# Performance work log

Hardware: AMD Instinct MI355X
Metric: run time of the kernel (lower is better)

The kernel has to match this reference:

```python
import jax, jax.numpy as jnp
import numpy as np

N, E, D, H = 50000, 800000, 128, 128


def _uniform_param(key, shape, fan_in):
    bound = 1.0 / np.sqrt(fan_in)
    return jax.random.uniform(key, shape, jnp.float32, -bound, bound)


def setup_inputs() -> dict:
    key = jax.random.key(0)
    ks = jax.random.split(key, 12)
    x = jax.random.normal(ks[0], (N, D), jnp.float32)
    xedge = jax.random.randint(ks[1], (2, E), 0, N, jnp.int64)
    y = jax.random.randint(ks[2], (N,), 0, 2, jnp.int32).astype(bool)
    return {
        "x": x,
        "xedge": xedge,
        "y": y,
        "pretrain": 0,
        # SAGEConv layer 1 (in=D, out=H): lin_l (with bias) applied to mean aggr, lin_r (no bias) to self
        "W1l": _uniform_param(ks[3], (D, H), D),
        "b1l": _uniform_param(ks[4], (H,), D),
        "W1r": _uniform_param(ks[5], (D, H), D),
        # SAGEConv layer 2 (in=H, out=H)
        "W2l": _uniform_param(ks[6], (H, H), H),
        "b2l": _uniform_param(ks[7], (H,), H),
        "W2r": _uniform_param(ks[8], (H, H), H),
        # Decoder weight [H, H]
        "Wdec": _uniform_param(ks[9], (H, H), H),
    }


def sage_conv(h, src, dst, Wl, bl, Wr, num_nodes):
    # gather neighbor features along edges, mean-aggregate by destination
    msgs = h[src]                                            # [E, d]
    agg = jax.ops.segment_sum(msgs, dst, num_segments=num_nodes)
    cnt = jax.ops.segment_sum(jnp.ones((src.shape[0],), h.dtype), dst,
                              num_segments=num_nodes)
    mean = agg / jnp.maximum(cnt, 1.0)[:, None]              # [N, d]
    return mean @ Wl + bl + h @ Wr                           # [N, out]


def reference(x, xedge, y, pretrain, W1l, b1l, W1r, W2l, b2l, W2r, Wdec):
    src, dst = xedge[0], xedge[1]
    n = x.shape[0]
    # Encoder: SAGE = conv1 -> relu -> (dropout: eval identity) -> conv2
    h = jax.nn.relu(sage_conv(x, src, dst, W1l, b1l, W1r, n))
    emb = sage_conv(h, src, dst, W2l, b2l, W2r, n)           # [N, H]
    # Decoder
    dx = emb @ Wdec                                          # [N, H]
    # BCEWithLogits: pos nodes target 1, neg nodes target 0, mean within each group
    ym = y.astype(dx.dtype)                                  # [N]
    n_pos = jnp.sum(ym)
    n_neg = n - n_pos
    hdim = dx.shape[1]
    sp_pos = jax.nn.softplus(-dx)   # bce(logit, 1)
    sp_neg = jax.nn.softplus(dx)    # bce(logit, 0)
    l2 = jnp.sum(sp_pos * ym[:, None]) / (jnp.maximum(n_pos, 1.0) * hdim)
    l1 = jnp.sum(sp_neg * (1.0 - ym)[:, None]) / (jnp.maximum(n_neg, 1.0) * hdim)
    return (l1 + l2, emb)
```

## Files before the change

kernel.cpp:

```cpp
#include <hip/hip_runtime.h>
#include <hip/hip_bf16.h>

#define NDIM 128
#define MROWS 32
#define BTHREADS 512
#define SCAN_CHUNK 1024

typedef __attribute__((ext_vector_type(8))) short short8;
typedef __attribute__((ext_vector_type(4))) float f32x4;

__device__ __forceinline__ float bf2f(__hip_bfloat16 v) { return __bfloat162float(v); }

__device__ __forceinline__ float ldf(const void* p, long i, int f32) {
    return f32 ? ((const float*)p)[i] : bf2f(((const __hip_bfloat16*)p)[i]);
}
__device__ __forceinline__ void stf(void* p, long i, int f32, float v) {
    if (f32) ((float*)p)[i] = v;
    else     ((__hip_bfloat16*)p)[i] = __float2bfloat16(v);
}
__device__ __forceinline__ short f2bf(float v) {
    __hip_bfloat16 h = __float2bfloat16(v);
    short s;
    __builtin_memcpy(&s, &h, 2);
    return s;
}
__device__ __forceinline__ float bflo(unsigned u) { u <<= 16; float f; __builtin_memcpy(&f, &u, 4); return f; }
__device__ __forceinline__ float bfhi(unsigned u) { u &= 0xffff0000u; float f; __builtin_memcpy(&f, &u, 4); return f; }
__device__ __forceinline__ unsigned packbf(float a, float b) {
    unsigned la = (unsigned short)f2bf(a);
    unsigned hb = (unsigned short)f2bf(b);
    return (hb << 16) | la;
}
__device__ __forceinline__ int aswz(int m, int k) {
    return m * NDIM + ((((k >> 3) ^ (m & 7)) << 3) | (k & 7));
}
__device__ __forceinline__ int wswz(int m, int p) {
    return m * 64 + ((((p >> 2) ^ (m & 7)) << 2) | (p & 3));
}

#define GLOAD(dst, sa, voff)                                              \
    asm volatile("global_load_dword %0, %1, %2"                           \
                 : "=v"(dst) : "v"(voff), "s"(sa) : "memory")


__global__ void prep_kernel(const void* __restrict__ x,
                            const void* __restrict__ W1l, const void* __restrict__ b1l,
                            const void* __restrict__ W1r, const void* __restrict__ W2l,
                            const void* __restrict__ b2l, const void* __restrict__ W2r,
                            const void* __restrict__ Wd,
                            short* __restrict__ T1l, short* __restrict__ T1r,
                            short* __restrict__ T2l, short* __restrict__ T2r,
                            short* __restrict__ Td, float* __restrict__ b1c,
                            float* __restrict__ b2c, unsigned* __restrict__ xb,
                            const int* __restrict__ xedge, int E,
                            int* __restrict__ cnt, int N,
                            int* __restrict__ flags) {
    __shared__ int s_se, s_sc;
    const int t = threadIdx.x;
    if (t == 0) { s_se = 1; s_sc = 0; }
    __syncthreads();
    {
        for (int i = t; i < 512; i += 256)
            if (xedge[2 * i + 1] != 0) s_se = 0;
        const unsigned short* xh = (const unsigned short*)x;
        int c = 0;
        for (int i = t; i < 1024; i += 256) {
            int ex = (xh[2 * i] >> 7) & 0xFF;
            if (ex >= 100 && ex <= 150) c++;
        }
        atomicAdd(&s_sc, c);
    }
    __syncthreads();
    const int e64 = s_se;
    const int wf = (s_sc < 900) ? 1 : 0;
    if (blockIdx.x == 0 && t == 0) {
        flags[0] = e64;
        flags[2] = wf;
    }
    const long idx = (long)blockIdx.x * 256 + t;
    if (idx < E) {
        int d = e64 ? xedge[2 * (E + idx)] : xedge[E + idx];
        atomicAdd(&cnt[d], 1);
    }
    if (idx < NDIM * NDIM) {
        int k = (int)(idx >> 7), n = (int)(idx & 127);
        int o = n * NDIM + k;
        T1l[o] = f2bf(ldf(W1l, idx, wf));
        T1r[o] = f2bf(ldf(W1r, idx, wf));
        T2l[o] = f2bf(ldf(W2l, idx, wf));
        T2r[o] = f2bf(ldf(W2r, idx, wf));
        Td [o] = f2bf(ldf(Wd , idx, wf));
        if (idx < NDIM) { b1c[idx] = ldf(b1l, idx, wf); b2c[idx] = ldf(b2l, idx, wf); }
    }
    if (wf) {
        const long np = (long)N * 64;
        const long stride = (long)gridDim.x * 256;
        for (long pidx = idx; pidx < np; pidx += stride) {
            float2 v = ((const float2*)x)[pidx];
            xb[pidx] = packbf(v.x, v.y);
        }
    }
}


__global__ void scan_partial(const int* __restrict__ cnt, int* __restrict__ bsum, int N,
                             const unsigned int* __restrict__ yw,
                             int* __restrict__ flags) {
    __shared__ int red[256];
    const int t = threadIdx.x;
    if (blockIdx.x == 0) {
        __shared__ int s_sy;
        if (t == 0) s_sy = 0;
        __syncthreads();
        for (int i = t; i < 1024; i += 256)
            if (yw[i] > 1u) s_sy = 1;
        __syncthreads();
        if (t == 0) flags[1] = s_sy;
    }
    const long base = (long)blockIdx.x * SCAN_CHUNK + (long)t * 4;
    int s = 0;
#pragma unroll
    for (int i = 0; i < 4; ++i) { long idx = base + i; if (idx < N) s += cnt[idx]; }
    red[t] = s;
    __syncthreads();
    for (int off = 128; off >= 1; off >>= 1) {
        if (t < off) red[t] += red[t + off];
        __syncthreads();
    }
    if (t == 0) bsum[blockIdx.x] = red[0];
}

__global__ void scan_scatter(int* __restrict__ cnt, const int* __restrict__ bsum,
                             int* __restrict__ rowptr, int N) {
    __shared__ int tsum[256];
    __shared__ int red[256];
    const int t = threadIdx.x;
    const long base = (long)blockIdx.x * SCAN_CHUNK + (long)t * 4;
    int loc[4];
    int s = 0;
#pragma unroll
    for (int i = 0; i < 4; ++i) {
        long idx = base + i;
        int c = (idx < N) ? cnt[idx] : 0;
        loc[i] = s;
        s += c;
    }
    tsum[t] = s;
    int sown = 0;
    for (int i = t; i < blockIdx.x; i += 256) sown += bsum[i];
    red[t] = sown;
    __syncthreads();
    for (int off = 1; off < 256; off <<= 1) {
        int u = (t >= off) ? tsum[t - off] : 0;
        __syncthreads();
        tsum[t] += u;
        __syncthreads();
    }
    for (int off = 128; off >= 1; off >>= 1) {
        if (t < off) red[t] += red[t + off];
        __syncthreads();
    }
    const int b0 = red[0];
    const int texcl = tsum[t] - s;
#pragma unroll
    for (int i = 0; i < 4; ++i) {
        long idx = base + i;
        if (idx < N) {
            int v = b0 + texcl + loc[i];
            rowptr[idx] = v;
            cnt[idx] = v;
        }
    }
    if (blockIdx.x == gridDim.x - 1 && t == 255) rowptr[N] = b0 + tsum[255];
}

__global__ void fill_kernel(const int* __restrict__ xedge, int E,
                            const int* __restrict__ flags,
                            int* __restrict__ cur, int* __restrict__ col) {
    int e = blockIdx.x * blockDim.x + threadIdx.x;
    if (e >= E) return;
    const int e64 = flags[0];
    int s = e64 ? xedge[2 * e] : xedge[e];
    int d = e64 ? xedge[2 * (E + e)] : xedge[E + e];
    int p = atomicAdd(&cur[d], 1);
    col[p] = s;
}


template <bool RELU, int OUTMODE>
__global__ __launch_bounds__(BTHREADS, 2)
void layer_mfma(const unsigned* __restrict__ Xb, const unsigned* __restrict__ Xraw,
                const int* __restrict__ rowptr,
                const int* __restrict__ col, const short* __restrict__ WlT,
                const float* __restrict__ biasc, const short* __restrict__ WrT,
                const short* __restrict__ WdT, const void* __restrict__ yv,
                const int* __restrict__ flags, void* __restrict__ outp,
                float* __restrict__ accum, int* __restrict__ npos, int N) {
    __shared__ short AS[2 * MROWS * NDIM];
    __shared__ int ylds[MROWS];
    __shared__ float redm[8][2];
    short* Ms = AS;
    short* Ss = AS + MROWS * NDIM;
    unsigned* Msw = (unsigned*)Ms;
    unsigned* Ssw = (unsigned*)Ss;
    const int t = threadIdx.x;
    const int n0 = blockIdx.x * MROWS;
    const int wf = flags[2];
    const unsigned* __restrict__ X = wf ? Xb : Xraw;

    if (OUTMODE == 1 && t < MROWS) {
        const int yb = flags[1];
        int n = n0 + t;
        int yn = -1;
        if (n < N)
            yn = yb ? (int)((const unsigned char*)yv)[n]
                    : (((const int*)yv)[n] != 0 ? 1 : 0);
        ylds[t] = yn;
    }

    {
        const int p = t & 63;
        const unsigned voff = (unsigned)(p * 4);
        const unsigned long long Xb64 = (unsigned long long)(uintptr_t)X;
        const int g = __builtin_amdgcn_readfirstlane(t >> 6);
        int r = g;
        int b = 0, e = 0;
        {
            int n = n0 + r;
            if (n < N) {
                b = __builtin_amdgcn_readfirstlane(rowptr[n]);
                e = __builtin_amdgcn_readfirstlane(rowptr[n + 1]);
            }
        }
        for (int it = 0; it < 4; ++it, r += 8) {
            const int n = n0 + r;
            const int deg = e - b;
            const int* colb = col + b;
            int cs[32];
            if (deg > 0) {
#pragma unroll
                for (int j = 0; j < 8; ++j) {
                    int c = __builtin_amdgcn_readfirstlane(colb[j]);
                    cs[j] = ((unsigned)c >= (unsigned)N) ? 0 : c;
                }
            }
            if (deg > 8) {
#pragma unroll
                for (int j = 8; j < 16; ++j) {
                    int c = __builtin_amdgcn_readfirstlane(colb[j]);
                    cs[j] = ((unsigned)c >= (unsigned)N) ? 0 : c;
                }
            }
            if (deg > 16) {
#pragma unroll
                for (int j = 16; j < 24; ++j) {
                    int c = __builtin_amdgcn_readfirstlane(colb[j]);
                    cs[j] = ((unsigned)c >= (unsigned)N) ? 0 : c;
                }
            }
            if (deg > 24) {
#pragma unroll
                for (int j = 24; j < 32; ++j) {
                    int c = __builtin_amdgcn_readfirstlane(colb[j]);
                    cs[j] = ((unsigned)c >= (unsigned)N) ? 0 : c;
                }
            }
            int bn = 0, en = 0;
            if (it < 3) {
                int nn = n0 + r + 8;
                if (nn < N) {
                    bn = __builtin_amdgcn_readfirstlane(rowptr[nn]);
                    en = __builtin_amdgcn_readfirstlane(rowptr[nn + 1]);
                }
            }
            unsigned u[32];
            unsigned su = 0;
            if (n < N) {
                unsigned long long sa = Xb64 + ((unsigned long long)(unsigned)n << 8);
                GLOAD(su, sa, voff);
            }
            if (deg > 0) {
#pragma unroll
                for (int j = 0; j < 8; ++j) {
                    unsigned long long sa = Xb64 + ((unsigned long long)(unsigned)cs[j] << 8);
                    GLOAD(u[j], sa, voff);
                }
            }
            if (deg > 8) {
#pragma unroll
                for (int j = 8; j < 16; ++j) {
                    unsigned long long sa = Xb64 + ((unsigned long long)(unsigned)cs[j] << 8);
                    GLOAD(u[j], sa, voff);
                }
            }
            if (deg > 16) {
#pragma unroll
                for (int j = 16; j < 24; ++j) {
                    unsigned long long sa = Xb64 + ((unsigned long long)(unsigned)cs[j] << 8);
                    GLOAD(u[j], sa, voff);
                }
            }
            if (deg > 24) {
#pragma unroll
                for (int j = 24; j < 32; ++j) {
                    unsigned long long sa = Xb64 + ((unsigned long long)(unsigned)cs[j] << 8);
                    GLOAD(u[j], sa, voff);
                }
            }
            asm volatile("s_waitcnt vmcnt(0)" ::: "memory");
            __builtin_amdgcn_sched_barrier(0);
            if (n < N) asm volatile("" : "+v"(su));
            if (deg > 0) {
#pragma unroll
                for (int j = 0; j < 8; ++j) asm volatile("" : "+v"(u[j]));
            }
            if (deg > 8) {
#pragma unroll
                for (int j = 8; j < 16; ++j) asm volatile("" : "+v"(u[j]));
            }
            if (deg > 16) {
#pragma unroll
                for (int j = 16; j < 24; ++j) asm volatile("" : "+v"(u[j]));
            }
            if (deg > 24) {
#pragma unroll
                for (int j = 24; j < 32; ++j) asm volatile("" : "+v"(u[j]));
            }
            float m0 = 0.f, m1 = 0.f;
            if (deg > 0) {
                float p0 = 0.f, p1 = 0.f, p2 = 0.f, p3 = 0.f;
                float q0 = 0.f, q1 = 0.f, q2 = 0.f, q3 = 0.f;
#pragma unroll
                for (int j = 0; j < 32; j += 4) {
                    if (j + 0 < deg) { p0 += bflo(u[j]);     q0 += bfhi(u[j]); }
                    if (j + 1 < deg) { p1 += bflo(u[j + 1]); q1 += bfhi(u[j + 1]); }
                    if (j + 2 < deg) { p2 += bflo(u[j + 2]); q2 += bfhi(u[j + 2]); }
                    if (j + 3 < deg) { p3 += bflo(u[j + 3]); q3 += bfhi(u[j + 3]); }
                }
                m0 = (p0 + p1) + (p2 + p3);
                m1 = (q0 + q1) + (q2 + q3);
                for (int i = b + 32; i < e; ++i) {
                    int c = __builtin_amdgcn_readfirstlane(col[i]);
                    unsigned uu = X[(long)c * 64 + p];
                    m0 += bflo(uu);
                    m1 += bfhi(uu);
                }
                float inv = 1.f / (float)deg;
                m0 *= inv; m1 *= inv;
            }
            int wi = wswz(r, p);
            Msw[wi] = packbf(m0, m1);
            Ssw[wi] = su;
            b = bn; e = en;
        }
    }
    __syncthreads();
    const int l = t & 63, w = t >> 6;
    const int quad = l >> 4, l15 = l & 15;
    const int wcol = w * 16;
    f32x4 acc[2] = {};
    for (int k0 = 0; k0 < NDIM; k0 += 32) {
        const int kc = k0 + quad * 8;
        short8 ams[2], ass[2], bl, br;
#pragma unroll
        for (int rt = 0; rt < 2; ++rt) {
            int m = rt * 16 + l15;
            ams[rt] = *(const short8*)&Ms[aswz(m, kc)];
            ass[rt] = *(const short8*)&Ss[aswz(m, kc)];
        }
        {
            int n = wcol + l15;
            bl = *(const short8*)&WlT[n * NDIM + kc];
            br = *(const short8*)&WrT[n * NDIM + kc];
        }
#pragma unroll
        for (int rt = 0; rt < 2; ++rt) {
            acc[rt] = __builtin_amdgcn_mfma_f32_16x16x32_bf16(
                ams[rt], bl, acc[rt], 0, 0, 0);
            acc[rt] = __builtin_amdgcn_mfma_f32_16x16x32_bf16(
                ass[rt], br, acc[rt], 0, 0, 0);
        }
    }
    __syncthreads();

    if (OUTMODE == 0) {
        {
            int cg = wcol + l15;
            float bv = biasc[cg];
#pragma unroll
            for (int rt = 0; rt < 2; ++rt)
#pragma unroll
                for (int reg = 0; reg < 4; ++reg) {
                    int row = rt * 16 + quad * 4 + reg;
                    float v = acc[rt][reg] + bv;
                    if (RELU) v = fmaxf(v, 0.f);
                    Ms[row * NDIM + cg] = f2bf(v);
                }
        }
        __syncthreads();
        unsigned* ob = (unsigned*)outp;
        for (int idx = t; idx < MROWS * 64; idx += BTHREADS) {
            int r = idx >> 6;
            if (n0 + r < N) ob[(long)n0 * 64 + idx] = Msw[idx];
        }
    } else {
        {
            int cg = wcol + l15;
            float bv = biasc[cg];
#pragma unroll
            for (int rt = 0; rt < 2; ++rt)
#pragma unroll
                for (int reg = 0; reg < 4; ++reg) {
                    int row = rt * 16 + quad * 4 + reg;
                    float v = acc[rt][reg] + bv;
                    Ms[aswz(row, cg)] = f2bf(v);
                    int n = n0 + row;
                    if (n < N) {
                        if (wf) ((float*)outp)[1 + (long)n * NDIM + cg] = v;
                        else ((__hip_bfloat16*)outp)[1 + (long)n * NDIM + cg] =
                                 __float2bfloat16(v);
                    }
                }
        }
        __syncthreads();
        f32x4 acc2[2] = {};
        for (int k0 = 0; k0 < NDIM; k0 += 32) {
            const int kc = k0 + quad * 8;
            short8 a[2], bwd;
#pragma unroll
            for (int rt = 0; rt < 2; ++rt)
                a[rt] = *(const short8*)&Ms[aswz(rt * 16 + l15, kc)];
            bwd = *(const short8*)&WdT[(wcol + l15) * NDIM + kc];
#pragma unroll
            for (int rt = 0; rt < 2; ++rt)
                acc2[rt] = __builtin_amdgcn_mfma_f32_16x16x32_bf16(
                    a[rt], bwd, acc2[rt], 0, 0, 0);
        }
        float lpos = 0.f, lneg = 0.f;
#pragma unroll
        for (int rt = 0; rt < 2; ++rt)
#pragma unroll
            for (int reg = 0; reg < 4; ++reg) {
                int row = rt * 16 + quad * 4 + reg;
                int yn = ylds[row];
                if (yn >= 0) {
                    float z = acc2[rt][reg];
                    float L = log1pf(expf(-fabsf(z)));
                    if (yn) lpos += fmaxf(-z, 0.f) + L;
                    else    lneg += fmaxf(z, 0.f) + L;
                }
            }
#pragma unroll
        for (int off = 32; off >= 1; off >>= 1) {
            lpos += __shfl_down(lpos, off, 64);
            lneg += __shfl_down(lneg, off, 64);
        }
        if (l == 0) { redm[w][0] = lpos; redm[w][1] = lneg; }
        __syncthreads();
        if (t == 0) {
            float sp = 0.f, sn = 0.f;
#pragma unroll
            for (int i = 0; i < 8; ++i) { sp += redm[i][0]; sn += redm[i][1]; }
            atomicAdd(&accum[0], sp);
            atomicAdd(&accum[1], sn);
            int c = 0;
            for (int i = 0; i < MROWS; ++i) if (ylds[i] > 0) c++;
            if (c) atomicAdd(npos, c);
        }
    }
}

__global__ void finalize_kernel(const float* __restrict__ accum, const int* __restrict__ npos,
                                const int* __restrict__ flags, void* __restrict__ out, int N) {
    float np_ = (float)(*npos);
    float nn_ = (float)N - np_;
    float l2 = accum[0] / (fmaxf(np_, 1.f) * 128.f);
    float l1 = accum[1] / (fmaxf(nn_, 1.f) * 128.f);
    stf(out, 0, flags[2], l1 + l2);
}


extern "C" void kernel_launch(void* const* d_in, const int* in_sizes, int n_in,
                              void* d_out, int out_size, void* d_ws, size_t ws_size,
                              hipStream_t stream) {
    const void* x    = d_in[0];
    const int* xedge = (const int*)d_in[1];
    const void* y    = d_in[2];
    const void* W1l  = d_in[4];
    const void* b1l  = d_in[5];
    const void* W1r  = d_in[6];
    const void* W2l  = d_in[7];
    const void* b2l  = d_in[8];
    const void* W2r  = d_in[9];
    const void* Wdec = d_in[10];

    const int N = in_sizes[0] / NDIM;
    const int E = in_sizes[1] / 2;

    char* ws = (char*)d_ws;
    size_t off = 0;
    auto alloc = [&](size_t bytes) -> void* {
        void* p = ws + off;
        off = (off + bytes + 255) & ~(size_t)255;
        return p;
    };
    int*   flags  = (int*)alloc(64);
    int*   cnt    = (int*)alloc((size_t)N * 4);
    float* accum  = (float*)alloc(64);
    int*   npos   = (int*)alloc(64);
    int*   bsum   = (int*)alloc(1024 * 4);
    int*   rowptr = (int*)alloc((size_t)(N + 1) * 4);
    int*   col    = (int*)alloc((size_t)E * 4);
    unsigned* xb  = (unsigned*)alloc((size_t)N * 64 * 4);
    unsigned* hbuf = (unsigned*)alloc((size_t)N * 64 * 4);
    short* T1l = (short*)alloc(NDIM * NDIM * 2);
    short* T1r = (short*)alloc(NDIM * NDIM * 2);
    short* T2l = (short*)alloc(NDIM * NDIM * 2);
    short* T2r = (short*)alloc(NDIM * NDIM * 2);
    short* Td  = (short*)alloc(NDIM * NDIM * 2);
    float* b1c = (float*)alloc(NDIM * 4);
    float* b2c = (float*)alloc(NDIM * 4);

    const size_t zlen = (((size_t)N * 4 + 255) & ~(size_t)255) + 512;
    hipMemsetAsync(cnt, 0, zlen, stream);

    const long prep_items = (E > NDIM * NDIM) ? E : NDIM * NDIM;
    prep_kernel<<<(int)((prep_items + 255) / 256), 256, 0, stream>>>(
        x, W1l, b1l, W1r, W2l, b2l, W2r, Wdec,
        T1l, T1r, T2l, T2r, Td, b1c, b2c, xb, xedge, E, cnt, N, flags);

    const int sb = (N + SCAN_CHUNK - 1) / SCAN_CHUNK;
    scan_partial<<<sb, 256, 0, stream>>>(cnt, bsum, N, (const unsigned int*)y, flags);
    scan_scatter<<<sb, 256, 0, stream>>>(cnt, bsum, rowptr, N);

    const int eb = (E + 255) / 256;
    fill_kernel<<<eb, 256, 0, stream>>>(xedge, E, flags, cnt, col);

    const int nbM = (N + MROWS - 1) / MROWS;
    layer_mfma<true, 0><<<nbM, BTHREADS, 0, stream>>>(
        xb, (const unsigned*)x, rowptr, col, T1l, b1c, T1r, nullptr, nullptr,
        flags, hbuf, nullptr, nullptr, N);
    layer_mfma<false, 1><<<nbM, BTHREADS, 0, stream>>>(
        hbuf, hbuf, rowptr, col, T2l, b2c, T2r, Td, y, flags,
        d_out, accum, npos, N);
    finalize_kernel<<<1, 1, 0, stream>>>(accum, npos, flags, d_out, N);
}
```

Baseline: 308.0 us.

## Fuse graph preprocessing into one cooperative kernel and fold finalize into last block

Replaces the memset, prep, two scan kernels and fill kernel with a single cooperative kernel of 1024 blocks. It uses grid-wide syncs between the degree-count, prefix-sum and CSR-fill phases. The separate finalize kernel is removed: the last block to finish the second layer, found through an atomic done counter, computes the loss. This cuts launch count and inter-kernel gaps, at the cost of grid.sync overhead, a serial per-block prefix loop, and relying on the cooperative launch succeeding (there is a fallback path).

```diff
diff --git a/kernel.cpp b/kernel.cpp
--- a/kernel.cpp
+++ b/kernel.cpp
@@ -1,10 +1,14 @@
 #include <hip/hip_runtime.h>
 #include <hip/hip_bf16.h>
+#include <hip/hip_cooperative_groups.h>
+
+namespace cg = cooperative_groups;
 
 #define NDIM 128
 #define MROWS 32
 #define BTHREADS 512
 #define SCAN_CHUNK 1024
+#define COOP_G 1024
 
 typedef __attribute__((ext_vector_type(8))) short short8;
 typedef __attribute__((ext_vector_type(4))) float f32x4;
@@ -41,6 +45,149 @@
 #define GLOAD(dst, sa, voff)                                              \
     asm volatile("global_load_dword %0, %1, %2"                           \
                  : "=v"(dst) : "v"(voff), "s"(sa) : "memory")
+
+__device__ __forceinline__ void detect_flags(const int* xedge, const void* x,
+                                             int* s_se, int* s_sc,
+                                             int* e64_out, int* wf_out) {
+    const int t = threadIdx.x;
+    if (t == 0) { *s_se = 1; *s_sc = 0; }
+    __syncthreads();
+    for (int i = t; i < 512; i += 256)
+        if (xedge[2 * i + 1] != 0) *s_se = 0;
+    {
+        const unsigned short* xh = (const unsigned short*)x;
+        int c = 0;
+        for (int i = t; i < 1024; i += 256) {
+            int ex = (xh[2 * i] >> 7) & 0xFF;
+            if (ex >= 100 && ex <= 150) c++;
+        }
+        atomicAdd(s_sc, c);
+    }
+    __syncthreads();
+    *e64_out = *s_se;
+    *wf_out = (*s_sc < 900) ? 1 : 0;
+}
+
+
+__global__ __launch_bounds__(256, 4)
+void coop_build(const void* __restrict__ x,
+                const void* __restrict__ W1l, const void* __restrict__ b1l,
+                const void* __restrict__ W1r, const void* __restrict__ W2l,
+                const void* __restrict__ b2l, const void* __restrict__ W2r,
+                const void* __restrict__ Wd,
+                short* __restrict__ T1l, short* __restrict__ T1r,
+                short* __restrict__ T2l, short* __restrict__ T2r,
+                short* __restrict__ Td, float* __restrict__ b1c,
+                float* __restrict__ b2c, unsigned* __restrict__ xb,
+                const int* __restrict__ xedge, int E,
+                int* __restrict__ cnt, int N,
+                int* __restrict__ flags, float* __restrict__ accum,
+                int* __restrict__ npos, int* __restrict__ donecnt,
+                int* __restrict__ gpart, int* __restrict__ rowptr,
+                int* __restrict__ col, const unsigned int* __restrict__ yw) {
+    cg::grid_group grid = cg::this_grid();
+    const int t = threadIdx.x;
+    const int b = blockIdx.x;
+    const long gid = (long)b * 256 + t;
+    const long gstride = (long)gridDim.x * 256;
+
+    __shared__ int s_se, s_sc;
+    int e64, wf;
+    detect_flags(xedge, x, &s_se, &s_sc, &e64, &wf);
+    if (b == 0) {
+        if (t == 0) {
+            flags[0] = e64; flags[2] = wf;
+            atomicExch((int*)&accum[0], 0);
+            atomicExch((int*)&accum[1], 0);
+            atomicExch(npos, 0);
+            atomicExch(donecnt, 0);
+        }
+        __shared__ int s_sy;
+        if (t == 0) s_sy = 0;
+        __syncthreads();
+        for (int i = t; i < 1024; i += 256)
+            if (yw[i] > 1u) s_sy = 1;
+        __syncthreads();
+        if (t == 0) flags[1] = s_sy;
+    }
+    for (long i = gid; i < N; i += gstride) atomicExch(&cnt[i], 0);
+    for (long i = gid; i < NDIM * NDIM; i += gstride) {
+        int k = (int)(i >> 7), n = (int)(i & 127);
+        int o = n * NDIM + k;
+        T1l[o] = f2bf(ldf(W1l, i, wf));
+        T1r[o] = f2bf(ldf(W1r, i, wf));
+        T2l[o] = f2bf(ldf(W2l, i, wf));
+        T2r[o] = f2bf(ldf(W2r, i, wf));
+        Td [o] = f2bf(ldf(Wd , i, wf));
+        if (i < NDIM) { b1c[i] = ldf(b1l, i, wf); b2c[i] = ldf(b2l, i, wf); }
+    }
+    if (wf) {
+        const long np = (long)N * 64;
+        for (long p = gid; p < np; p += gstride) {
+            float2 v = ((const float2*)x)[p];
+            xb[p] = packbf(v.x, v.y);
+        }
+    }
+    grid.sync();
+    for (long e = gid; e < E; e += gstride) {
+        int d = e64 ? xedge[2 * (E + e)] : xedge[E + e];
+        atomicAdd(&cnt[d], 1);
+    }
+    grid.sync();
+    const int C = (N + gridDim.x - 1) / gridDim.x;
+    __shared__ int red[256];
+    __shared__ int sc_[1024];
+    {
+        int s = 0;
+        for (int i = t; i < C; i += 256) {
+            long idx = (long)b * C + i;
+            if (idx < N) s += atomicAdd(&cnt[idx], 0);
+        }
+        red[t] = s;
+        __syncthreads();
+        for (int off = 128; off >= 1; off >>= 1) {
+            if (t < off) red[t] += red[t + off];
+            __syncthreads();
+        }
+        if (t == 0) atomicExch(&gpart[b], red[0]);
+    }
+    grid.sync();
+    {
+        int sown = 0;
+        for (int i = t; i < b; i += 256) sown += atomicAdd(&gpart[i], 0);
+        red[t] = sown;
+        __syncthreads();
+        for (int off = 128; off >= 1; off >>= 1) {
+            if (t < off) red[t] += red[t + off];
+            __syncthreads();
+        }
+        const int base = red[0];
+        for (int i = t; i < C; i += 256) {
+            long idx = (long)b * C + i;
+            sc_[i] = (idx < N) ? atomicAdd(&cnt[idx], 0) : 0;
+        }
+        __syncthreads();
+        if (t == 0) {
+            int run = base;
+            for (int i = 0; i < C; ++i) {
+                long idx = (long)b * C + i;
+                if (idx < N) {
+                    rowptr[idx] = run;
+                    atomicExch(&cnt[idx], run);
+                    run += sc_[i];
+                }
+            }
+        }
+        if (b == 0 && t == 0) rowptr[N] = E;
+    }
+    grid.sync();
+    for (long e = gid; e < E; e += gstride) {
+        int s_ = e64 ? xedge[2 * e] : xedge[e];
+        int d  = e64 ? xedge[2 * (E + e)] : xedge[E + e];
+        int p = atomicAdd(&cnt[d], 1);
+        col[p] = s_;
+    }
+}
 
 
 __global__ void prep_kernel(const void* __restrict__ x,
@@ -57,26 +204,9 @@
                             int* __restrict__ flags) {
     __shared__ int s_se, s_sc;
     const int t = threadIdx.x;
-    if (t == 0) { s_se = 1; s_sc = 0; }
-    __syncthreads();
-    {
-        for (int i = t; i < 512; i += 256)
-            if (xedge[2 * i + 1] != 0) s_se = 0;
-        const unsigned short* xh = (const unsigned short*)x;
-        int c = 0;
-        for (int i = t; i < 1024; i += 256) {
-            int ex = (xh[2 * i] >> 7) & 0xFF;
-            if (ex >= 100 && ex <= 150) c++;
-        }
-        atomicAdd(&s_sc, c);
-    }
-    __syncthreads();
-    const int e64 = s_se;
-    const int wf = (s_sc < 900) ? 1 : 0;
-    if (blockIdx.x == 0 && t == 0) {
-        flags[0] = e64;
-        flags[2] = wf;
-    }
+    int e64, wf;
+    detect_flags(xedge, x, &s_se, &s_sc, &e64, &wf);
+    if (blockIdx.x == 0 && t == 0) { flags[0] = e64; flags[2] = wf; }
     const long idx = (long)blockIdx.x * 256 + t;
     if (idx < E) {
         int d = e64 ? xedge[2 * (E + idx)] : xedge[E + idx];
@@ -101,7 +231,6 @@
         }
     }
 }
-
 
 __global__ void scan_partial(const int* __restrict__ cnt, int* __restrict__ bsum, int N,
                              const unsigned int* __restrict__ yw,
@@ -195,7 +324,8 @@
                 const float* __restrict__ biasc, const short* __restrict__ WrT,
                 const short* __restrict__ WdT, const void* __restrict__ yv,
                 const int* __restrict__ flags, void* __restrict__ outp,
-                float* __restrict__ accum, int* __restrict__ npos, int N) {
+                float* __restrict__ accum, int* __restrict__ npos,
+                int* __restrict__ donecnt, int N) {
     __shared__ short AS[2 * MROWS * NDIM];
     __shared__ int ylds[MROWS];
     __shared__ float redm[8][2];
@@ -466,17 +596,20 @@
             int c = 0;
             for (int i = 0; i < MROWS; ++i) if (ylds[i] > 0) c++;
             if (c) atomicAdd(npos, c);
-        }
-    }
-}
-
-__global__ void finalize_kernel(const float* __restrict__ accum, const int* __restrict__ npos,
-                                const int* __restrict__ flags, void* __restrict__ out, int N) {
-    float np_ = (float)(*npos);
-    float nn_ = (float)N - np_;
-    float l2 = accum[0] / (fmaxf(np_, 1.f) * 128.f);
-    float l1 = accum[1] / (fmaxf(nn_, 1.f) * 128.f);
-    stf(out, 0, flags[2], l1 + l2);
+            __threadfence();
+            unsigned d = (unsigned)atomicAdd(donecnt, 1);
+            if (d == (unsigned)(gridDim.x - 1)) {
+                float spT = atomicAdd(&accum[0], 0.f);
+                float snT = atomicAdd(&accum[1], 0.f);
+                int npv = atomicAdd(npos, 0);
+                float np_ = (float)npv;
+                float nn_ = (float)N - np_;
+                float l2v = spT / (fmaxf(np_, 1.f) * 128.f);
+                float l1v = snT / (fmaxf(nn_, 1.f) * 128.f);
+                stf(outp, 0, wf, l1v + l2v);
+            }
+        }
+    }
 }
 
 
@@ -508,7 +641,8 @@
     int*   cnt    = (int*)alloc((size_t)N * 4);
     float* accum  = (float*)alloc(64);
     int*   npos   = (int*)alloc(64);
-    int*   bsum   = (int*)alloc(1024 * 4);
+    int*   donecnt= (int*)alloc(64);
+    int*   gpart  = (int*)alloc((size_t)COOP_G * 4);
     int*   rowptr = (int*)alloc((size_t)(N + 1) * 4);
     int*   col    = (int*)alloc((size_t)E * 4);
     unsigned* xb  = (unsigned*)alloc((size_t)N * 64 * 4);
@@ -521,27 +655,42 @@
     float* b1c = (float*)alloc(NDIM * 4);
     float* b2c = (float*)alloc(NDIM * 4);
 
-    const size_t zlen = (((size_t)N * 4 + 255) & ~(size_t)255) + 512;
-    hipMemsetAsync(cnt, 0, zlen, stream);
-
-    const long prep_items = (E > NDIM * NDIM) ? E : NDIM * NDIM;
-    prep_kernel<<<(int)((prep_items + 255) / 256), 256, 0, stream>>>(
-        x, W1l, b1l, W1r, W2l, b2l, W2r, Wdec,
-        T1l, T1r, T2l, T2r, Td, b1c, b2c, xb, xedge, E, cnt, N, flags);
-
-    const int sb = (N + SCAN_CHUNK - 1) / SCAN_CHUNK;
-    scan_partial<<<sb, 256, 0, stream>>>(cnt, bsum, N, (const unsigned int*)y, flags);
-    scan_scatter<<<sb, 256, 0, stream>>>(cnt, bsum, rowptr, N);
-
-    const int eb = (E + 255) / 256;
-    fill_kernel<<<eb, 256, 0, stream>>>(xedge, E, flags, cnt, col);
+    bool coop_ok = (N <= COOP_G * 1024);
+    if (coop_ok) {
+        const void* xv = x;
+        int Ev = E, Nv = N;
+        void* args[] = {
+            (void*)&xv, (void*)&W1l, (void*)&b1l, (void*)&W1r, (void*)&W2l,
+            (void*)&b2l, (void*)&W2r, (void*)&Wdec,
+            (void*)&T1l, (void*)&T1r, (void*)&T2l, (void*)&T2r, (void*)&Td,
+            (void*)&b1c, (void*)&b2c, (void*)&xb, (void*)&xedge, (void*)&Ev,
+            (void*)&cnt, (void*)&Nv, (void*)&flags, (void*)&accum,
+            (void*)&npos, (void*)&donecnt, (void*)&gpart, (void*)&rowptr,
+            (void*)&col, (void*)&y };
+        hipError_t err = hipLaunchCooperativeKernel(
+            (const void*)coop_build, dim3(COOP_G), dim3(256), args, 0, stream);
+        if (err != hipSuccess) coop_ok = false;
+    }
+    if (!coop_ok) {
+        const size_t zlen = (((size_t)N * 4 + 255) & ~(size_t)255) + 3 * 256;
+        hipMemsetAsync(cnt, 0, zlen, stream);
+        const long prep_items = (E > NDIM * NDIM) ? E : NDIM * NDIM;
+        prep_kernel<<<(int)((prep_items + 255) / 256), 256, 0, stream>>>(
+            x, W1l, b1l, W1r, W2l, b2l, W2r, Wdec,
+            T1l, T1r, T2l, T2r, Td, b1c, b2c, xb, xedge, E, cnt, N, flags);
+        const int sb = (N + SCAN_CHUNK - 1) / SCAN_CHUNK;
+        scan_partial<<<sb, 256, 0, stream>>>(cnt, gpart, N,
+                                             (const unsigned int*)y, flags);
+        scan_scatter<<<sb, 256, 0, stream>>>(cnt, gpart, rowptr, N);
+        const int eb = (E + 255) / 256;
+        fill_kernel<<<eb, 256, 0, stream>>>(xedge, E, flags, cnt, col);
+    }
 
     const int nbM = (N + MROWS - 1) / MROWS;
     layer_mfma<true, 0><<<nbM, BTHREADS, 0, stream>>>(
         xb, (const unsigned*)x, rowptr, col, T1l, b1c, T1r, nullptr, nullptr,
-        flags, hbuf, nullptr, nullptr, N);
+        flags, hbuf, nullptr, nullptr, nullptr, N);
     layer_mfma<false, 1><<<nbM, BTHREADS, 0, stream>>>(
         hbuf, hbuf, rowptr, col, T2l, b2c, T2r, Td, y, flags,
-        d_out, accum, npos, N);
-    finalize_kernel<<<1, 1, 0, stream>>>(accum, npos, flags, d_out, N);
-}
+        d_out, accum, npos, donecnt, N);
+}
```

New measurement: 816.4 us. 165% more time.
